# Optimization experiments

Hardware: AMD Instinct MI355X
Metric: run time of the kernel (lower is better)

## Reference

```python
import jax, jax.numpy as jnp
import numpy as np

N_POINTS = 300000
NUM_CLUSTERS = 64
LATENT_DIM = 32
DET = 1e-16  # matches `det` in update_gamma


def setup_inputs() -> dict:
    key = jax.random.key(0)
    k1, k2, k3 = jax.random.split(key, 3)
    mu_phi = jax.random.normal(k1, (N_POINTS, LATENT_DIM), dtype=jnp.float32)
    # per-node scalar log-variance (encoder's gcn_logstddev has output dim 1)
    log_cov_phi = jax.random.normal(k2, (N_POINTS, 1), dtype=jnp.float32) * 0.1
    pi_k = jnp.ones((NUM_CLUSTERS,), jnp.float32) / NUM_CLUSTERS
    mu_k = jax.random.normal(k3, (NUM_CLUSTERS, LATENT_DIM), dtype=jnp.float32)
    log_cov_k = jnp.full((NUM_CLUSTERS, 1), 0.1, jnp.float32)
    return {"mu_phi": mu_phi, "log_cov_phi": log_cov_phi, "pi_k": pi_k,
            "mu_k": mu_k, "log_cov_k": log_cov_k, "P": LATENT_DIM}


def _sq_dist(a, b):
    # ||a_i - b_k||^2 via expansion; avoids materializing [N,K,P]
    return (jnp.sum(a * a, axis=1)[:, None]
            - 2.0 * (a @ b.T)
            + jnp.sum(b * b, axis=1)[None, :])


def reference(mu_phi, log_cov_phi, pi_k, mu_k, log_cov_k, P):
    Pf = jnp.float32(P)
    lcp = log_cov_phi[:, 0]          # [N]
    lck = log_cov_k[:, 0]            # [K]
    # --- update_gamma: KL[i,k] between q(z_i) and cluster k (isotropic) ---
    sq = _sq_dist(mu_phi, mu_k)      # [N,K]
    inv_cov_k = jnp.exp(-lck)[None, :]
    KL = 0.5 * (Pf * (lck[None, :] - lcp[:, None]) - Pf
                + Pf * jnp.exp(lcp)[:, None] * inv_cov_k
                + sq * inv_cov_k)    # [N,K]
    w = pi_k[None, :] * jnp.exp(-KL)
    gamma = w / jnp.sum(w, axis=1, keepdims=True) + DET  # [N,K]
    # --- update_others: M-step using the new gamma ---
    N_k = jnp.sum(gamma, axis=0)                          # [K]
    pi_new = N_k / jnp.float32(gamma.shape[0])
    mu_new = (gamma.T @ mu_phi) / N_k[:, None]            # [K,P]
    sq2 = _sq_dist(mu_phi, mu_new)                        # [N,K]
    diff = Pf * jnp.exp(lcp)[:, None] + sq2               # [N,K]
    cov_new = jnp.sum(gamma * diff, axis=0) / (Pf * N_k)  # [K]
    log_cov_new = jnp.log(cov_new)[:, None]               # [K,1]
    return gamma, pi_new, mu_new, log_cov_new
```

## Files before the change

kernel.cpp:

```cpp
#include <hip/hip_runtime.h>
#include <math.h>

#define N_POINTS 300000
#define K 64
#define P 32
#define DETC 1e-16f

#define WS_FLOATS (K + K + K * P)

#define NBLOCKS 1280
#define NTHREADS 256

__global__ __launch_bounds__(NTHREADS) void em_pass(
    const float* __restrict__ mu_phi,
    const float* __restrict__ log_cov_phi,
    const float* __restrict__ pi_k,
    const float* __restrict__ mu_k,
    const float* __restrict__ log_cov_k,
    float* __restrict__ gamma_out,
    float* __restrict__ ws)
{
    const int lane = threadIdx.x & 63;
    const int wave = __builtin_amdgcn_readfirstlane(threadIdx.x >> 6);
    const int wavesPerBlock = NTHREADS >> 6;
    const int gw = blockIdx.x * wavesPerBlock + wave;
    const int W  = gridDim.x * wavesPerBlock;

    float muk[P];
#pragma unroll
    for (int d = 0; d < P; ++d) muk[d] = mu_k[lane * P + d];
    const float lck  = log_cov_k[lane];
    const float icov = __expf(-lck);
    const float pik  = pi_k[lane];
    float n2k = 0.f;
#pragma unroll
    for (int d = 0; d < P; ++d) n2k = fmaf(muk[d], muk[d], n2k);

    float accN = 0.f, accS = 0.f;
    float accM[P];
#pragma unroll
    for (int d = 0; d < P; ++d) accM[d] = 0.f;

    const float Pf = (float)P;

    for (int i = gw; i < N_POINTS; i += W) {
        const float4* row4 = reinterpret_cast<const float4*>(mu_phi) + (size_t)i * (P / 4);
        float m[P];
#pragma unroll
        for (int j = 0; j < P / 4; ++j) {
            float4 v = row4[j];
            m[4 * j + 0] = v.x; m[4 * j + 1] = v.y;
            m[4 * j + 2] = v.z; m[4 * j + 3] = v.w;
        }
        const float lcp = log_cov_phi[i];

        float dot = 0.f, n2i = 0.f;
#pragma unroll
        for (int d = 0; d < P; ++d) {
            dot = fmaf(m[d], muk[d], dot);
            n2i = fmaf(m[d], m[d], n2i);
        }
        const float sq   = n2i - 2.f * dot + n2k;
        const float elcp = __expf(lcp);
        const float KL   = 0.5f * (Pf * (lck - lcp) - Pf + Pf * elcp * icov + sq * icov);
        const float w    = pik * __expf(-KL);

        float sw = w;
#pragma unroll
        for (int off = 32; off; off >>= 1) sw += __shfl_xor(sw, off, 64);

        const float g = w * __builtin_amdgcn_rcpf(sw) + DETC;
        gamma_out[(size_t)i * K + lane] = g;

        accN += g;
        accS  = fmaf(g, fmaf(Pf, elcp, n2i), accS);
#pragma unroll
        for (int d = 0; d < P; ++d) accM[d] = fmaf(g, m[d], accM[d]);
    }

    __shared__ float lN[K], lS[K], lM[K * P];
    for (int idx = threadIdx.x; idx < K; idx += NTHREADS) { lN[idx] = 0.f; lS[idx] = 0.f; }
    for (int idx = threadIdx.x; idx < K * P; idx += NTHREADS) lM[idx] = 0.f;
    __syncthreads();

    atomicAdd(&lN[lane], accN);
    atomicAdd(&lS[lane], accS);
#pragma unroll
    for (int d = 0; d < P; ++d) atomicAdd(&lM[d * K + lane], accM[d]);
    __syncthreads();

    for (int idx = threadIdx.x; idx < K; idx += NTHREADS) {
        atomicAdd(&ws[idx], lN[idx]);
        atomicAdd(&ws[K + idx], lS[idx]);
    }
    for (int idx = threadIdx.x; idx < K * P; idx += NTHREADS)
        atomicAdd(&ws[2 * K + idx], lM[idx]);
}

__global__ void finalize(const float* __restrict__ ws, float* __restrict__ out_tail)
{
    const int k = threadIdx.x;
    if (k >= K) return;
    const float Nk = ws[k];
    const float S  = ws[K + k];
    float* pi_new      = out_tail;
    float* mu_new      = out_tail + K;
    float* log_cov_new = out_tail + K + K * P;

    pi_new[k] = Nk / (float)N_POINTS;

    const float invN = 1.f / Nk;
    float m2 = 0.f;
#pragma unroll
    for (int d = 0; d < P; ++d) {
        const float m = ws[2 * K + d * K + k] * invN;
        mu_new[k * P + d] = m;
        m2 = fmaf(m, m, m2);
    }
    const float cov = (S - Nk * m2) / ((float)P * Nk);
    log_cov_new[k] = logf(cov);
}

extern "C" void kernel_launch(void* const* d_in, const int* in_sizes, int n_in,
                              void* d_out, int out_size, void* d_ws, size_t ws_size,
                              hipStream_t stream)
{
    const float* mu_phi      = (const float*)d_in[0];
    const float* log_cov_phi = (const float*)d_in[1];
    const float* pi_k        = (const float*)d_in[2];
    const float* mu_k        = (const float*)d_in[3];
    const float* log_cov_k   = (const float*)d_in[4];
    float* out = (float*)d_out;
    float* ws  = (float*)d_ws;

    hipMemsetAsync(ws, 0, WS_FLOATS * sizeof(float), stream);
    em_pass<<<NBLOCKS, NTHREADS, 0, stream>>>(mu_phi, log_cov_phi, pi_k, mu_k,
                                              log_cov_k, out, ws);
    finalize<<<1, 64, 0, stream>>>(ws, out + (size_t)N_POINTS * K);
}
```

Before: 235.3 us.

## Fuse finalize via last-block reduction, batch per-point norms, use DPP reductions

Each wave now takes a contiguous chunk of points. Row norms and log-covariances are computed lane-parallel for 64 points at a time and then broadcast with readlane. Per-cluster constants are folded into a single KL offset, and the cross-lane sum uses DPP row operations plus readlanes instead of shfl_xor. The finalize kernel is merged into em_pass through a last-block-done atomic counter, which removes one launch at the cost of an extra fence and counter. Launch bounds and block count are also changed, and rows are read from scalar-uniform addresses, which may use scalar loads.

```diff
diff --git a/kernel.cpp b/kernel.cpp
--- a/kernel.cpp
+++ b/kernel.cpp
@@ -1,30 +1,38 @@
 #include <hip/hip_runtime.h>
 #include <math.h>
 
-#define N_POINTS 300000
+#define NPTS 300000
 #define K 64
 #define P 32
 #define DETC 1e-16f
-
 #define WS_FLOATS (K + K + K * P)
 
-#define NBLOCKS 1280
+#define NBLOCKS 1024
 #define NTHREADS 256
+#define NWAVES (NBLOCKS * (NTHREADS / 64))
+#define CHUNK ((NPTS + NWAVES - 1) / NWAVES)
 
-__global__ __launch_bounds__(NTHREADS) void em_pass(
+#define DPP_ADD(v, ctrl)                                                     \
+    v += __int_as_float(__builtin_amdgcn_update_dpp(                         \
+        0, __float_as_int(v), (ctrl), 0xF, 0xF, true))
+
+__device__ __forceinline__ float rl(float x, int lane) {
+    return __int_as_float(__builtin_amdgcn_readlane(__float_as_int(x), lane));
+}
+
+__global__ __launch_bounds__(NTHREADS, 4) void em_pass(
     const float* __restrict__ mu_phi,
     const float* __restrict__ log_cov_phi,
     const float* __restrict__ pi_k,
     const float* __restrict__ mu_k,
     const float* __restrict__ log_cov_k,
     float* __restrict__ gamma_out,
+    float* __restrict__ out_tail,
     float* __restrict__ ws)
 {
     const int lane = threadIdx.x & 63;
-    const int wave = __builtin_amdgcn_readfirstlane(threadIdx.x >> 6);
-    const int wavesPerBlock = NTHREADS >> 6;
-    const int gw = blockIdx.x * wavesPerBlock + wave;
-    const int W  = gridDim.x * wavesPerBlock;
+    const int wave = threadIdx.x >> 6;
+    const int gw = __builtin_amdgcn_readfirstlane(blockIdx.x * (NTHREADS / 64) + wave);
 
     float muk[P];
 #pragma unroll
@@ -35,47 +43,65 @@
     float n2k = 0.f;
 #pragma unroll
     for (int d = 0; d < P; ++d) n2k = fmaf(muk[d], muk[d], n2k);
+    const float Ak    = 0.5f * (32.f * lck - 32.f + icov * n2k) - __logf(pik);
+    const float hicov = 0.5f * icov;
 
     float accN = 0.f, accS = 0.f;
     float accM[P];
 #pragma unroll
     for (int d = 0; d < P; ++d) accM[d] = 0.f;
 
-    const float Pf = (float)P;
+    const int start = gw * CHUNK;
+    const int end0  = (start + CHUNK < NPTS) ? (start + CHUNK) : NPTS;
 
-    for (int i = gw; i < N_POINTS; i += W) {
-        const float4* row4 = reinterpret_cast<const float4*>(mu_phi) + (size_t)i * (P / 4);
-        float m[P];
+    for (int gb = start; gb < end0; gb += 64) {
+        const int cnt = (end0 - gb < 64) ? (end0 - gb) : 64;
+
+        float u_v = 0.f, lcp_v = 0.f;
+        const int ip = gb + lane;
+        if (lane < cnt) {
+            const float4* r4 = reinterpret_cast<const float4*>(mu_phi + (size_t)ip * P);
+            float4 a0 = r4[0], a1 = r4[1], a2 = r4[2], a3 = r4[3];
+            float4 a4 = r4[4], a5 = r4[5], a6 = r4[6], a7 = r4[7];
+            float n2 = 0.f;
+#define N2ACC(q) n2 = fmaf(q.x,q.x,n2); n2 = fmaf(q.y,q.y,n2); \
+                 n2 = fmaf(q.z,q.z,n2); n2 = fmaf(q.w,q.w,n2)
+            N2ACC(a0); N2ACC(a1); N2ACC(a2); N2ACC(a3);
+            N2ACC(a4); N2ACC(a5); N2ACC(a6); N2ACC(a7);
+#undef N2ACC
+            lcp_v = log_cov_phi[ip];
+            u_v   = fmaf(32.f, __expf(lcp_v), n2);
+        }
+
+#pragma unroll 2
+        for (int p = 0; p < cnt; ++p) {
+            const int i = gb + p;
+            const float u_s    = rl(u_v, p);
+            const float base_s = 16.f * rl(lcp_v, p);
+            const float* row = mu_phi + (size_t)i * P;
+
+            float dot = 0.f;
 #pragma unroll
-        for (int j = 0; j < P / 4; ++j) {
-            float4 v = row4[j];
-            m[4 * j + 0] = v.x; m[4 * j + 1] = v.y;
-            m[4 * j + 2] = v.z; m[4 * j + 3] = v.w;
+            for (int d = 0; d < P; ++d) dot = fmaf(row[d], muk[d], dot);
+
+            const float t = fmaf(-hicov, u_s, base_s) - Ak;
+            const float w = __expf(fmaf(icov, dot, t));
+
+            float v = w;
+            DPP_ADD(v, 0xB1);
+            DPP_ADD(v, 0x4E);
+            DPP_ADD(v, 0x128);
+            DPP_ADD(v, 0x124);
+            const float sum = (rl(v, 0) + rl(v, 16)) + (rl(v, 32) + rl(v, 48));
+
+            const float g = fmaf(w, __builtin_amdgcn_rcpf(sum), DETC);
+            gamma_out[(size_t)i * K + lane] = g;
+
+            accN += g;
+            accS  = fmaf(g, u_s, accS);
+#pragma unroll
+            for (int d = 0; d < P; ++d) accM[d] = fmaf(g, row[d], accM[d]);
         }
-        const float lcp = log_cov_phi[i];
-
-        float dot = 0.f, n2i = 0.f;
-#pragma unroll
-        for (int d = 0; d < P; ++d) {
-            dot = fmaf(m[d], muk[d], dot);
-            n2i = fmaf(m[d], m[d], n2i);
-        }
-        const float sq   = n2i - 2.f * dot + n2k;
-        const float elcp = __expf(lcp);
-        const float KL   = 0.5f * (Pf * (lck - lcp) - Pf + Pf * elcp * icov + sq * icov);
-        const float w    = pik * __expf(-KL);
-
-        float sw = w;
-#pragma unroll
-        for (int off = 32; off; off >>= 1) sw += __shfl_xor(sw, off, 64);
-
-        const float g = w * __builtin_amdgcn_rcpf(sw) + DETC;
-        gamma_out[(size_t)i * K + lane] = g;
-
-        accN += g;
-        accS  = fmaf(g, fmaf(Pf, elcp, n2i), accS);
-#pragma unroll
-        for (int d = 0; d < P; ++d) accM[d] = fmaf(g, m[d], accM[d]);
     }
 
     __shared__ float lN[K], lS[K], lM[K * P];
@@ -95,30 +121,39 @@
     }
     for (int idx = threadIdx.x; idx < K * P; idx += NTHREADS)
         atomicAdd(&ws[2 * K + idx], lM[idx]);
-}
+    __syncthreads();
 
-__global__ void finalize(const float* __restrict__ ws, float* __restrict__ out_tail)
-{
-    const int k = threadIdx.x;
-    if (k >= K) return;
-    const float Nk = ws[k];
-    const float S  = ws[K + k];
-    float* pi_new      = out_tail;
-    float* mu_new      = out_tail + K;
-    float* log_cov_new = out_tail + K + K * P;
+    __shared__ int lastf;
+    if (threadIdx.x == 0) {
+        __threadfence();
+        const int c = atomicAdd((int*)(ws + WS_FLOATS), 1);
+        lastf = (c == NBLOCKS - 1);
+    }
+    __syncthreads();
+    if (lastf) {
+        __threadfence();
+        const int k = threadIdx.x;
+        if (k < K) {
+            const float Nk = __hip_atomic_load(&ws[k],     __ATOMIC_RELAXED, __HIP_MEMORY_SCOPE_AGENT);
+            const float S  = __hip_atomic_load(&ws[K + k], __ATOMIC_RELAXED, __HIP_MEMORY_SCOPE_AGENT);
+            float* pi_new      = out_tail;
+            float* mu_new      = out_tail + K;
+            float* log_cov_new = out_tail + K + K * P;
 
-    pi_new[k] = Nk / (float)N_POINTS;
-
-    const float invN = 1.f / Nk;
-    float m2 = 0.f;
+            pi_new[k] = Nk / (float)NPTS;
+            const float invN = 1.f / Nk;
+            float m2 = 0.f;
 #pragma unroll
-    for (int d = 0; d < P; ++d) {
-        const float m = ws[2 * K + d * K + k] * invN;
-        mu_new[k * P + d] = m;
-        m2 = fmaf(m, m, m2);
+            for (int d = 0; d < P; ++d) {
+                const float md = __hip_atomic_load(&ws[2 * K + d * K + k],
+                                                   __ATOMIC_RELAXED, __HIP_MEMORY_SCOPE_AGENT) * invN;
+                mu_new[k * P + d] = md;
+                m2 = fmaf(md, md, m2);
+            }
+            const float cov = (S - Nk * m2) / (32.f * Nk);
+            log_cov_new[k] = logf(cov);
+        }
     }
-    const float cov = (S - Nk * m2) / ((float)P * Nk);
-    log_cov_new[k] = logf(cov);
 }
 
 extern "C" void kernel_launch(void* const* d_in, const int* in_sizes, int n_in,
@@ -133,8 +168,8 @@
     float* out = (float*)d_out;
     float* ws  = (float*)d_ws;
 
-    hipMemsetAsync(ws, 0, WS_FLOATS * sizeof(float), stream);
+    hipMemsetAsync(ws, 0, (WS_FLOATS + 1) * sizeof(float), stream);
     em_pass<<<NBLOCKS, NTHREADS, 0, stream>>>(mu_phi, log_cov_phi, pi_k, mu_k,
-                                              log_cov_k, out, ws);
-    finalize<<<1, 64, 0, stream>>>(ws, out + (size_t)N_POINTS * K);
+                                              log_cov_k, out,
+                                              out + (size_t)NPTS * K, ws);
 }
```

After: 203.7 us. 1.16x faster.
